# Optimization experiments

Hardware: AMD Instinct MI355X
Metric: run time of the kernel (lower is better)

## Reference

```python
import jax, jax.numpy as jnp
import numpy as np

B, T, N, H, P = 16, 64, 512, 128, 12


def _laplacian_with_self_loop(adj):
    a = adj + jnp.eye(adj.shape[0], dtype=adj.dtype)
    d_inv_sqrt = 1.0 / jnp.sqrt(a.sum(axis=1))
    return a * d_inv_sqrt[:, None] * d_inv_sqrt[None, :]


def setup_inputs() -> dict:
    key = jax.random.key(0)
    ks = jax.random.split(key, 10)
    inputs = jax.random.normal(ks[0], (B, T, N), dtype=jnp.float32)
    adj = jax.random.uniform(ks[1], (N, N), dtype=jnp.float32)
    adj = (adj + adj.T) * 0.5
    laplacian = _laplacian_with_self_loop(adj)

    def xavier(k, shape):
        fan_in, fan_out = shape[0], shape[1]
        lim = np.sqrt(6.0 / (fan_in + fan_out))
        return jax.random.uniform(k, shape, jnp.float32, -lim, lim)

    W1 = xavier(ks[2], (H + 1, 2 * H))      # graph_conv1 weights
    b1 = jnp.ones((2 * H,), jnp.float32)    # bias init 1.0
    W2 = xavier(ks[3], (H + 1, H))          # graph_conv2 weights
    b2 = jnp.zeros((H,), jnp.float32)
    att_w1 = xavier(ks[4], (H, 1))
    att_w2 = xavier(ks[5], (N, 1))
    att_w3 = xavier(ks[6], (N, 1))
    att_b1 = jnp.zeros((1,), jnp.float32)
    att_b2 = jnp.zeros((1,), jnp.float32)
    att_b3 = jnp.zeros((1,), jnp.float32)
    W_out = xavier(ks[7], (T, P))
    b_out = jnp.zeros((P,), jnp.float32)
    return dict(inputs=inputs, laplacian=laplacian, W1=W1, b1=b1, W2=W2, b2=b2,
                att_w1=att_w1, att_w2=att_w2, att_w3=att_w3,
                att_b1=att_b1, att_b2=att_b2, att_b3=att_b3,
                W_out=W_out, b_out=b_out)


def reference(inputs, laplacian, W1, b1, W2, b2,
              att_w1, att_w2, att_w3, att_b1, att_b2, att_b3,
              W_out, b_out):
    Bs, Ts, Ns = inputs.shape
    Hs = W2.shape[1]

    def graph_conv(x_t, h_flat, W, b):
        # x_t: [B,N]; h_flat: [B, N*H]
        h = h_flat.reshape(Bs, Ns, Hs)
        conc = jnp.concatenate([x_t[..., None], h], axis=-1)     # [B,N,H+1]
        agg = jnp.einsum('mn,bnc->bmc', laplacian, conc)          # [B,N,H+1]
        out = agg @ W + b                                         # [B,N,O]
        return out.reshape(Bs, -1)                                # [B,N*O] (flattened, matching torch)

    def step(h_flat, x_t):
        ru = jax.nn.sigmoid(graph_conv(x_t, h_flat, W1, b1))      # [B, N*2H]
        r, u = jnp.split(ru, 2, axis=1)                            # split on flattened dim (faithful)
        c = jnp.tanh(graph_conv(x_t, r * h_flat, W2, b2))          # [B, N*H]
        new_h = u * h_flat + (1.0 - u) * c
        return new_h, new_h

    h0 = jnp.zeros((Bs, Ns * Hs), inputs.dtype)
    _, hs = jax.lax.scan(step, h0, jnp.moveaxis(inputs, 1, 0))     # [T,B,N*H]
    hidden_states = jnp.moveaxis(hs, 0, 1).reshape(Bs, Ts, Ns, Hs)

    # SelfAttention: project H->1, then N->1 per (b,t), softmax over T
    hs1 = hidden_states.reshape(-1, Hs) @ att_w1 + att_b1          # [B*T*N, 1]
    f = (hs1.reshape(-1, Ns) @ att_w2 + att_b2).reshape(Bs, Ts)
    g = (hs1.reshape(-1, Ns) @ att_w3 + att_b3).reshape(Bs, Ts)
    beta = jax.nn.softmax(g * f, axis=-1)                          # [B,T]
    context = beta[:, :, None] * hs1.reshape(Bs, Ts, Ns)           # [B,T,N]

    context = context.transpose(0, 2, 1)                           # [B,N,T]
    Ps = W_out.shape[1]
    out = (context.reshape(-1, Ts) @ W_out + b_out).reshape(Bs, Ns, Ps)
    return out.transpose(0, 2, 1)                                  # [B,pre_len,N]
```

## Files before the change

### kernel.cpp

```cpp
#include <hip/hip_runtime.h>
#include <math.h>

#define B_ 16
#define T_ 64
#define N_ 512
#define H_ 128
#define P_ 12
#define NH 65536

__global__ __launch_bounds__(512) void lx_kernel(const float* __restrict__ x,
                                                 const float* __restrict__ L,
                                                 float* __restrict__ Lx) {
    __shared__ __align__(16) float xs[2][N_];
    const int r0 = blockIdx.x * 2;
    const int tid = threadIdx.x;
    for (int j = 0; j < 2; ++j)
        xs[j][tid] = x[(size_t)(r0 + j) * N_ + tid];
    __syncthreads();
    float a0 = 0.f, a1 = 0.f;
    const int m = tid;
#pragma unroll 8
    for (int n = 0; n < N_; ++n) {
        float lv = L[(size_t)n * N_ + m];
        a0 += xs[0][n] * lv;
        a1 += xs[1][n] * lv;
    }
    Lx[(size_t)(r0 + 0) * N_ + m] = a0;
    Lx[(size_t)(r0 + 1) * N_ + m] = a1;
}

#define FMA4(dst, a, hv)                                                      \
    dst[0] += (a) * (hv).x; dst[1] += (a) * (hv).y;                           \
    dst[2] += (a) * (hv).z; dst[3] += (a) * (hv).w;

__global__ __launch_bounds__(512) void gc1_kernel(
    const float* __restrict__ L, const float* __restrict__ Hprev,
    const float* __restrict__ Lx, const float* __restrict__ W1,
    const float* __restrict__ b1, float* __restrict__ rh,
    float* __restrict__ u, int t) {
    __shared__ __align__(16) float Ht[2][32][H_];
    union LW {
        float Lt[2][32][20];
        float Wt[16][260];
    };
    __shared__ __align__(16) LW sm;
    __shared__ __align__(16) float Zb[16][H_];

    const int tid = threadIdx.x;
    const int b = blockIdx.x & 15;
    const int m0 = (blockIdx.x >> 4) * 16;
    const float* __restrict__ Hb = Hprev + (size_t)b * NH;

    const int hrow = tid >> 5, hcol = (tid & 31) * 4;
    const int lm = tid >> 5, lk = tid & 31;

    {
        *(float4*)&Ht[0][hrow][hcol] = *(const float4*)&Hb[(size_t)hrow * H_ + hcol];
        *(float4*)&Ht[0][hrow + 16][hcol] =
            *(const float4*)&Hb[(size_t)(hrow + 16) * H_ + hcol];
        sm.Lt[0][lk][lm] = L[(size_t)(m0 + lm) * N_ + lk];
    }
    __syncthreads();

    const int g = tid >> 6;
    const int l = tid & 63;
    const int ty = l >> 4;
    const int tx = l & 15;
    const int ma0 = ty * 4;
    const int ca0 = tx * 4, cb0 = 64 + tx * 4;

    float acc[4][2][4] = {};

    for (int kc = 0; kc < 16; ++kc) {
        const int bi = kc & 1, bj = bi ^ 1;
        float4 p0, p1;
        float pl;
        if (kc < 15) {
            const size_t kb = (size_t)(kc + 1) * 32;
            p0 = *(const float4*)&Hb[(kb + hrow) * H_ + hcol];
            p1 = *(const float4*)&Hb[(kb + hrow + 16) * H_ + hcol];
            pl = L[(size_t)(m0 + lm) * N_ + kb + lk];
        }
#pragma unroll
        for (int kk = 0; kk < 4; ++kk) {
            const int k = g * 4 + kk;
            const float4 la = *(const float4*)&sm.Lt[bi][k][ma0];
            const float4 h0 = *(const float4*)&Ht[bi][k][ca0];
            const float4 h1 = *(const float4*)&Ht[bi][k][cb0];
            FMA4(acc[0][0], la.x, h0) FMA4(acc[0][1], la.x, h1)
            FMA4(acc[1][0], la.y, h0) FMA4(acc[1][1], la.y, h1)
            FMA4(acc[2][0], la.z, h0) FMA4(acc[2][1], la.z, h1)
            FMA4(acc[3][0], la.w, h0) FMA4(acc[3][1], la.w, h1)
        }
        if (kc < 15) {
            *(float4*)&Ht[bj][hrow][hcol] = p0;
            *(float4*)&Ht[bj][hrow + 16][hcol] = p1;
            sm.Lt[bj][lk][lm] = pl;
        }
        __syncthreads();
    }

    for (int r = 0; r < 8; ++r) {
        if (g == r) {
#pragma unroll
            for (int i = 0; i < 4; ++i) {
#pragma unroll
                for (int v = 0; v < 2; ++v) {
                    const int c = v ? cb0 : ca0;
                    float4* zp = (float4*)&Zb[ma0 + i][c];
                    if (r == 0) {
                        *zp = make_float4(acc[i][v][0], acc[i][v][1],
                                          acc[i][v][2], acc[i][v][3]);
                    } else {
                        float4 z = *zp;
                        *zp = make_float4(z.x + acc[i][v][0], z.y + acc[i][v][1],
                                          z.z + acc[i][v][2], z.w + acc[i][v][3]);
                    }
                }
            }
        }
        __syncthreads();
    }

    const int to = tid & 63, tm = tid >> 6;
    const int o0 = to * 4;
    float a2[2][4] = {};
    const int wr = tid >> 5, wc = (tid & 31) * 4;

    for (int ck = 0; ck < 8; ++ck) {
        *(float4*)&sm.Wt[wr][wc] =
            *(const float4*)&W1[(size_t)(1 + ck * 16 + wr) * 256 + wc];
        *(float4*)&sm.Wt[wr][wc + 128] =
            *(const float4*)&W1[(size_t)(1 + ck * 16 + wr) * 256 + wc + 128];
        __syncthreads();
#pragma unroll
        for (int ch4 = 0; ch4 < 4; ++ch4) {
            const float4 w0v = *(const float4*)&sm.Wt[ch4 * 4 + 0][o0];
            const float4 w1v = *(const float4*)&sm.Wt[ch4 * 4 + 1][o0];
            const float4 w2v = *(const float4*)&sm.Wt[ch4 * 4 + 2][o0];
            const float4 w3v = *(const float4*)&sm.Wt[ch4 * 4 + 3][o0];
            const int cc = ck * 16 + ch4 * 4;
#pragma unroll
            for (int i = 0; i < 2; ++i) {
                const float4 zv = *(const float4*)&Zb[tm + 8 * i][cc];
                a2[i][0] += zv.x * w0v.x + zv.y * w1v.x + zv.z * w2v.x + zv.w * w3v.x;
                a2[i][1] += zv.x * w0v.y + zv.y * w1v.y + zv.z * w2v.y + zv.w * w3v.y;
                a2[i][2] += zv.x * w0v.z + zv.y * w1v.z + zv.z * w2v.z + zv.w * w3v.z;
                a2[i][3] += zv.x * w0v.w + zv.y * w1v.w + zv.z * w2v.w + zv.w * w3v.w;
            }
        }
        __syncthreads();
    }

    const float4 w0r = *(const float4*)&W1[o0];
    const float4 bbv = *(const float4*)&b1[o0];
    const float* __restrict__ LxRow = Lx + ((size_t)b * T_ + t) * N_ + m0;
    float* __restrict__ rhB = rh + (size_t)b * NH;
    float* __restrict__ uB = u + (size_t)b * NH;
    const bool isR = (m0 < 256);
#pragma unroll
    for (int i = 0; i < 2; ++i) {
        const int mi = tm + 8 * i;
        const float lx = LxRow[mi];
        float v0 = a2[i][0] + lx * w0r.x + bbv.x;
        float v1 = a2[i][1] + lx * w0r.y + bbv.y;
        float v2 = a2[i][2] + lx * w0r.z + bbv.z;
        float v3 = a2[i][3] + lx * w0r.w + bbv.w;
        float s0 = 1.f / (1.f + expf(-v0));
        float s1 = 1.f / (1.f + expf(-v1));
        float s2 = 1.f / (1.f + expf(-v2));
        float s3 = 1.f / (1.f + expf(-v3));
        const int fl = (m0 + mi) * 256 + o0;
        if (isR) {
            float4 hv = *(const float4*)&Hb[fl];
            *(float4*)&rhB[fl] = make_float4(s0 * hv.x, s1 * hv.y, s2 * hv.z, s3 * hv.w);
        } else {
            *(float4*)&uB[fl - NH] = make_float4(s0, s1, s2, s3);
        }
    }
}

__global__ __launch_bounds__(512) void gc2a_kernel(
    const float* __restrict__ L, const float* __restrict__ rh,
    float* __restrict__ Z) {
    __shared__ __align__(16) float Ht[2][32][H_];
    __shared__ __align__(16) float Lt[2][32][20];
    __shared__ __align__(16) float Zb[16][H_];

    const int tid = threadIdx.x;
    const int b = blockIdx.x & 15;
    const int m0 = (blockIdx.x >> 4) * 16;
    const float* __restrict__ Rb = rh + (size_t)b * NH;

    const int hrow = tid >> 5, hcol = (tid & 31) * 4;
    const int lm = tid >> 5, lk = tid & 31;

    {
        *(float4*)&Ht[0][hrow][hcol] = *(const float4*)&Rb[(size_t)hrow * H_ + hcol];
        *(float4*)&Ht[0][hrow + 16][hcol] =
            *(const float4*)&Rb[(size_t)(hrow + 16) * H_ + hcol];
        Lt[0][lk][lm] = L[(size_t)(m0 + lm) * N_ + lk];
    }
    __syncthreads();

    const int g = tid >> 6;
    const int l = tid & 63;
    const int ty = l >> 4;
    const int tx = l & 15;
    const int ma0 = ty * 4;
    const int ca0 = tx * 4, cb0 = 64 + tx * 4;

    float acc[4][2][4] = {};

    for (int kc = 0; kc < 16; ++kc) {
        const int bi = kc & 1, bj = bi ^ 1;
        float4 p0, p1;
        float pl;
        if (kc < 15) {
            const size_t kb = (size_t)(kc + 1) * 32;
            p0 = *(const float4*)&Rb[(kb + hrow) * H_ + hcol];
            p1 = *(const float4*)&Rb[(kb + hrow + 16) * H_ + hcol];
            pl = L[(size_t)(m0 + lm) * N_ + kb + lk];
        }
#pragma unroll
        for (int kk = 0; kk < 4; ++kk) {
            const int k = g * 4 + kk;
            const float4 la = *(const float4*)&Lt[bi][k][ma0];
            const float4 h0 = *(const float4*)&Ht[bi][k][ca0];
            const float4 h1 = *(const float4*)&Ht[bi][k][cb0];
            FMA4(acc[0][0], la.x, h0) FMA4(acc[0][1], la.x, h1)
            FMA4(acc[1][0], la.y, h0) FMA4(acc[1][1], la.y, h1)
            FMA4(acc[2][0], la.z, h0) FMA4(acc[2][1], la.z, h1)
            FMA4(acc[3][0], la.w, h0) FMA4(acc[3][1], la.w, h1)
        }
        if (kc < 15) {
            *(float4*)&Ht[bj][hrow][hcol] = p0;
            *(float4*)&Ht[bj][hrow + 16][hcol] = p1;
            Lt[bj][lk][lm] = pl;
        }
        __syncthreads();
    }

    for (int r = 0; r < 8; ++r) {
        if (g == r) {
#pragma unroll
            for (int i = 0; i < 4; ++i) {
#pragma unroll
                for (int v = 0; v < 2; ++v) {
                    const int c = v ? cb0 : ca0;
                    float4* zp = (float4*)&Zb[ma0 + i][c];
                    if (r == 0) {
                        *zp = make_float4(acc[i][v][0], acc[i][v][1],
                                          acc[i][v][2], acc[i][v][3]);
                    } else {
                        float4 z = *zp;
                        *zp = make_float4(z.x + acc[i][v][0], z.y + acc[i][v][1],
                                          z.z + acc[i][v][2], z.w + acc[i][v][3]);
                    }
                }
            }
        }
        __syncthreads();
    }

    {
        const int zr = tid >> 5, zc = (tid & 31) * 4;
        *(float4*)&Z[((size_t)b * NH) + (size_t)(m0 + zr) * H_ + zc] =
            *(const float4*)&Zb[zr][zc];
    }
}

__global__ __launch_bounds__(256) void gc2b_kernel(
    const float* __restrict__ Hprev, const float* __restrict__ u,
    const float* __restrict__ Lx, const float* __restrict__ W2,
    const float* __restrict__ b2, const float* __restrict__ aw1,
    const float* __restrict__ ab1, float* __restrict__ Hnew,
    float* __restrict__ hs1, int t) {
    __shared__ __align__(16) float Zs[8][H_];
    __shared__ __align__(16) float Wt[16][H_];

    const int tid = threadIdx.x;
    const int b = blockIdx.x & 15;
    const int m0 = (blockIdx.x >> 4) * 8;
    const size_t gbase = (size_t)b * NH + (size_t)m0 * H_;

    const int row = tid >> 5;
    const int o0 = (tid & 31) * 4;

    *(float4*)&Zs[row][o0] = *(const float4*)&Hnew[gbase + (size_t)row * H_ + o0];

    float a2[4] = {0.f, 0.f, 0.f, 0.f};

#pragma unroll 1
    for (int ck = 0; ck < 8; ++ck) {
        __syncthreads();
        *(float4*)&Wt[row][o0] =
            *(const float4*)&W2[(size_t)(1 + ck * 16 + row) * H_ + o0];
        *(float4*)&Wt[row + 8][o0] =
            *(const float4*)&W2[(size_t)(1 + ck * 16 + row + 8) * H_ + o0];
        __syncthreads();
#pragma unroll
        for (int ch4 = 0; ch4 < 4; ++ch4) {
            const float4 w0v = *(const float4*)&Wt[ch4 * 4 + 0][o0];
            const float4 w1v = *(const float4*)&Wt[ch4 * 4 + 1][o0];
            const float4 w2v = *(const float4*)&Wt[ch4 * 4 + 2][o0];
            const float4 w3v = *(const float4*)&Wt[ch4 * 4 + 3][o0];
            const float4 zv = *(const float4*)&Zs[row][ck * 16 + ch4 * 4];
            a2[0] += zv.x * w0v.x + zv.y * w1v.x + zv.z * w2v.x + zv.w * w3v.x;
            a2[1] += zv.x * w0v.y + zv.y * w1v.y + zv.z * w2v.y + zv.w * w3v.y;
            a2[2] += zv.x * w0v.z + zv.y * w1v.z + zv.z * w2v.z + zv.w * w3v.z;
            a2[3] += zv.x * w0v.w + zv.y * w1v.w + zv.z * w2v.w + zv.w * w3v.w;
        }
    }

    const float4 w0r = *(const float4*)&W2[o0];
    const float4 bbv = *(const float4*)&b2[o0];
    const float4 awv = *(const float4*)&aw1[o0];
    const int m = m0 + row;
    const float lx = Lx[((size_t)b * T_ + t) * N_ + m];

    float c0 = tanhf(a2[0] + lx * w0r.x + bbv.x);
    float c1 = tanhf(a2[1] + lx * w0r.y + bbv.y);
    float c2 = tanhf(a2[2] + lx * w0r.z + bbv.z);
    float c3 = tanhf(a2[3] + lx * w0r.w + bbv.w);

    const size_t fl = gbase + (size_t)row * H_ + o0;
    const float4 uv = *(const float4*)&u[fl];
    const float4 hp = *(const float4*)&Hprev[fl];
    const float h0 = uv.x * hp.x + (1.f - uv.x) * c0;
    const float h1 = uv.y * hp.y + (1.f - uv.y) * c1;
    const float h2 = uv.z * hp.z + (1.f - uv.z) * c2;
    const float h3 = uv.w * hp.w + (1.f - uv.w) * c3;
    *(float4*)&Hnew[fl] = make_float4(h0, h1, h2, h3);

    float part = h0 * awv.x + h1 * awv.y + h2 * awv.z + h3 * awv.w;
#pragma unroll
    for (int off = 16; off; off >>= 1) part += __shfl_xor(part, off);
    if ((tid & 31) == 0)
        hs1[((size_t)b * T_ + t) * N_ + m] = part + ab1[0];
}

__global__ __launch_bounds__(64) void att_beta_kernel(
    const float* __restrict__ hs1, const float* __restrict__ aw2,
    const float* __restrict__ aw3, const float* __restrict__ ab2,
    const float* __restrict__ ab3, float* __restrict__ beta) {
    const int b = blockIdx.x;
    const int t = threadIdx.x;
    const float* __restrict__ row = hs1 + ((size_t)b * T_ + t) * N_;
    float f = 0.f, g = 0.f;
    for (int n = 0; n < N_; n += 4) {
        float4 hv = *(const float4*)&row[n];
        float4 w2v = *(const float4*)&aw2[n];
        float4 w3v = *(const float4*)&aw3[n];
        f += hv.x * w2v.x + hv.y * w2v.y + hv.z * w2v.z + hv.w * w2v.w;
        g += hv.x * w3v.x + hv.y * w3v.y + hv.z * w3v.z + hv.w * w3v.w;
    }
    f += ab2[0];
    g += ab3[0];
    float s = f * g;
    float mx = s;
    for (int off = 32; off; off >>= 1) mx = fmaxf(mx, __shfl_xor(mx, off));
    float e = expf(s - mx);
    float sum = e;
    for (int off = 32; off; off >>= 1) sum += __shfl_xor(sum, off);
    beta[b * T_ + t] = e / sum;
}

__global__ __launch_bounds__(256) void att_out_kernel(
    const float* __restrict__ hs1, const float* __restrict__ beta,
    const float* __restrict__ Wout, const float* __restrict__ bout,
    float* __restrict__ out) {
    __shared__ float bs[T_];
    __shared__ float ws[T_][P_];
    const int b = blockIdx.x;
    const int tid = threadIdx.x;
    if (tid < T_) bs[tid] = beta[b * T_ + tid];
    for (int i = tid; i < T_ * P_; i += 256) ws[i / P_][i % P_] = Wout[i];
    __syncthreads();
    for (int nn = 0; nn < 2; ++nn) {
        const int n = tid + nn * 256;
        float acc[P_];
#pragma unroll
        for (int p = 0; p < P_; ++p) acc[p] = bout[p];
        for (int t = 0; t < T_; ++t) {
            float v = bs[t] * hs1[((size_t)b * T_ + t) * N_ + n];
#pragma unroll
            for (int p = 0; p < P_; ++p) acc[p] += v * ws[t][p];
        }
#pragma unroll
        for (int p = 0; p < P_; ++p) out[((size_t)b * P_ + p) * N_ + n] = acc[p];
    }
}

extern "C" void kernel_launch(void* const* d_in, const int* in_sizes, int n_in,
                              void* d_out, int out_size, void* d_ws, size_t ws_size,
                              hipStream_t stream) {
    const float* x = (const float*)d_in[0];
    const float* L = (const float*)d_in[1];
    const float* W1 = (const float*)d_in[2];
    const float* b1 = (const float*)d_in[3];
    const float* W2 = (const float*)d_in[4];
    const float* b2 = (const float*)d_in[5];
    const float* aw1 = (const float*)d_in[6];
    const float* aw2 = (const float*)d_in[7];
    const float* aw3 = (const float*)d_in[8];
    const float* ab1 = (const float*)d_in[9];
    const float* ab2 = (const float*)d_in[10];
    const float* ab3 = (const float*)d_in[11];
    const float* Wout = (const float*)d_in[12];
    const float* bout = (const float*)d_in[13];
    float* out = (float*)d_out;

    float* ws = (float*)d_ws;
    float* Lx = ws;
    float* hs1 = Lx + B_ * T_ * N_;
    float* hb0 = hs1 + B_ * T_ * N_;
    float* hb1 = hb0 + (size_t)B_ * NH;
    float* rh = hb1 + (size_t)B_ * NH;
    float* u = rh + (size_t)B_ * NH;
    float* beta = u + (size_t)B_ * NH;
    (void)in_sizes; (void)n_in; (void)out_size; (void)ws_size;

    hipMemsetAsync(hb0, 0, (size_t)B_ * NH * sizeof(float), stream);
    lx_kernel<<<512, 512, 0, stream>>>(x, L, Lx);

    for (int t = 0; t < T_; ++t) {
        float* hp = (t & 1) ? hb1 : hb0;
        float* hn = (t & 1) ? hb0 : hb1;
        gc1_kernel<<<512, 512, 0, stream>>>(L, hp, Lx, W1, b1, rh, u, t);
        gc2a_kernel<<<512, 512, 0, stream>>>(L, rh, hn);
        gc2b_kernel<<<1024, 256, 0, stream>>>(hp, u, Lx, W2, b2, aw1, ab1,
                                              hn, hs1, t);
    }
    att_beta_kernel<<<16, 64, 0, stream>>>(hs1, aw2, aw3, ab2, ab3, beta);
    att_out_kernel<<<16, 256, 0, stream>>>(hs1, beta, Wout, bout, out);
}
```

Baseline: 4.001 ms.

## Reorder second graph conv as L·(rh·W2) and fuse the GRU epilogue

The second graph convolution now multiplies r*h by W2 first, in a new per-node kernel, and then applies the Laplacian to the result. This lets the Laplacian GEMM kernel finish with the tanh, GRU update and attention projection directly from shared memory. The intermediate Z no longer makes a global round trip, and the Laplacian GEMM's output feeds the epilogue directly, at the cost of an extra Y buffer. A padding shared array is added, which appears meant to limit occupancy or change the LDS footprint.

```diff
diff --git a/kernel.cpp b/kernel.cpp
--- a/kernel.cpp
+++ b/kernel.cpp
@@ -180,25 +180,77 @@
     }
 }
 
-__global__ __launch_bounds__(512) void gc2a_kernel(
-    const float* __restrict__ L, const float* __restrict__ rh,
-    float* __restrict__ Z) {
+__global__ __launch_bounds__(256) void y_kernel(
+    const float* __restrict__ rh, const float* __restrict__ W2,
+    float* __restrict__ Y) {
+    __shared__ __align__(16) float Zs[8][H_];
+    __shared__ __align__(16) float Wt[16][H_];
+
+    const int tid = threadIdx.x;
+    const int b = blockIdx.x & 15;
+    const int n0 = (blockIdx.x >> 4) * 8;
+    const size_t gbase = (size_t)b * NH + (size_t)n0 * H_;
+
+    const int row = tid >> 5;
+    const int o0 = (tid & 31) * 4;
+
+    *(float4*)&Zs[row][o0] = *(const float4*)&rh[gbase + (size_t)row * H_ + o0];
+
+    float a2[4] = {0.f, 0.f, 0.f, 0.f};
+
+#pragma unroll 1
+    for (int ck = 0; ck < 8; ++ck) {
+        __syncthreads();
+        *(float4*)&Wt[row][o0] =
+            *(const float4*)&W2[(size_t)(1 + ck * 16 + row) * H_ + o0];
+        *(float4*)&Wt[row + 8][o0] =
+            *(const float4*)&W2[(size_t)(1 + ck * 16 + row + 8) * H_ + o0];
+        __syncthreads();
+#pragma unroll
+        for (int ch4 = 0; ch4 < 4; ++ch4) {
+            const float4 w0v = *(const float4*)&Wt[ch4 * 4 + 0][o0];
+            const float4 w1v = *(const float4*)&Wt[ch4 * 4 + 1][o0];
+            const float4 w2v = *(const float4*)&Wt[ch4 * 4 + 2][o0];
+            const float4 w3v = *(const float4*)&Wt[ch4 * 4 + 3][o0];
+            const float4 zv = *(const float4*)&Zs[row][ck * 16 + ch4 * 4];
+            a2[0] += zv.x * w0v.x + zv.y * w1v.x + zv.z * w2v.x + zv.w * w3v.x;
+            a2[1] += zv.x * w0v.y + zv.y * w1v.y + zv.z * w2v.y + zv.w * w3v.y;
+            a2[2] += zv.x * w0v.z + zv.y * w1v.z + zv.z * w2v.z + zv.w * w3v.z;
+            a2[3] += zv.x * w0v.w + zv.y * w1v.w + zv.z * w2v.w + zv.w * w3v.w;
+        }
+    }
+
+    *(float4*)&Y[gbase + (size_t)row * H_ + o0] =
+        make_float4(a2[0], a2[1], a2[2], a2[3]);
+}
+
+__global__ __launch_bounds__(512) void gcz_kernel(
+    const float* __restrict__ L, const float* __restrict__ Y,
+    const float* __restrict__ Hprev, const float* __restrict__ u,
+    const float* __restrict__ Lx, const float* __restrict__ W2,
+    const float* __restrict__ b2, const float* __restrict__ aw1,
+    const float* __restrict__ ab1, float* __restrict__ Hnew,
+    float* __restrict__ hs1, int t) {
     __shared__ __align__(16) float Ht[2][32][H_];
     __shared__ __align__(16) float Lt[2][32][20];
     __shared__ __align__(16) float Zb[16][H_];
+    __shared__ __align__(16) float pad_[2880];
 
     const int tid = threadIdx.x;
+    if (tid < 16) pad_[tid] = 0.f;
+    asm volatile("" ::: "memory");
+
     const int b = blockIdx.x & 15;
     const int m0 = (blockIdx.x >> 4) * 16;
-    const float* __restrict__ Rb = rh + (size_t)b * NH;
+    const float* __restrict__ Yb = Y + (size_t)b * NH;
 
     const int hrow = tid >> 5, hcol = (tid & 31) * 4;
     const int lm = tid >> 5, lk = tid & 31;
 
     {
-        *(float4*)&Ht[0][hrow][hcol] = *(const float4*)&Rb[(size_t)hrow * H_ + hcol];
+        *(float4*)&Ht[0][hrow][hcol] = *(const float4*)&Yb[(size_t)hrow * H_ + hcol];
         *(float4*)&Ht[0][hrow + 16][hcol] =
-            *(const float4*)&Rb[(size_t)(hrow + 16) * H_ + hcol];
+            *(const float4*)&Yb[(size_t)(hrow + 16) * H_ + hcol];
         Lt[0][lk][lm] = L[(size_t)(m0 + lm) * N_ + lk];
     }
     __syncthreads();
@@ -218,8 +270,8 @@
         float pl;
         if (kc < 15) {
             const size_t kb = (size_t)(kc + 1) * 32;
-            p0 = *(const float4*)&Rb[(kb + hrow) * H_ + hcol];
-            p1 = *(const float4*)&Rb[(kb + hrow + 16) * H_ + hcol];
+            p0 = *(const float4*)&Yb[(kb + hrow) * H_ + hcol];
+            p1 = *(const float4*)&Yb[(kb + hrow + 16) * H_ + hcol];
             pl = L[(size_t)(m0 + lm) * N_ + kb + lk];
         }
 #pragma unroll
@@ -263,68 +315,20 @@
         __syncthreads();
     }
 
-    {
-        const int zr = tid >> 5, zc = (tid & 31) * 4;
-        *(float4*)&Z[((size_t)b * NH) + (size_t)(m0 + zr) * H_ + zc] =
-            *(const float4*)&Zb[zr][zc];
-    }
-}
-
-__global__ __launch_bounds__(256) void gc2b_kernel(
-    const float* __restrict__ Hprev, const float* __restrict__ u,
-    const float* __restrict__ Lx, const float* __restrict__ W2,
-    const float* __restrict__ b2, const float* __restrict__ aw1,
-    const float* __restrict__ ab1, float* __restrict__ Hnew,
-    float* __restrict__ hs1, int t) {
-    __shared__ __align__(16) float Zs[8][H_];
-    __shared__ __align__(16) float Wt[16][H_];
-
-    const int tid = threadIdx.x;
-    const int b = blockIdx.x & 15;
-    const int m0 = (blockIdx.x >> 4) * 8;
-    const size_t gbase = (size_t)b * NH + (size_t)m0 * H_;
-
-    const int row = tid >> 5;
-    const int o0 = (tid & 31) * 4;
-
-    *(float4*)&Zs[row][o0] = *(const float4*)&Hnew[gbase + (size_t)row * H_ + o0];
-
-    float a2[4] = {0.f, 0.f, 0.f, 0.f};
-
-#pragma unroll 1
-    for (int ck = 0; ck < 8; ++ck) {
-        __syncthreads();
-        *(float4*)&Wt[row][o0] =
-            *(const float4*)&W2[(size_t)(1 + ck * 16 + row) * H_ + o0];
-        *(float4*)&Wt[row + 8][o0] =
-            *(const float4*)&W2[(size_t)(1 + ck * 16 + row + 8) * H_ + o0];
-        __syncthreads();
-#pragma unroll
-        for (int ch4 = 0; ch4 < 4; ++ch4) {
-            const float4 w0v = *(const float4*)&Wt[ch4 * 4 + 0][o0];
-            const float4 w1v = *(const float4*)&Wt[ch4 * 4 + 1][o0];
-            const float4 w2v = *(const float4*)&Wt[ch4 * 4 + 2][o0];
-            const float4 w3v = *(const float4*)&Wt[ch4 * 4 + 3][o0];
-            const float4 zv = *(const float4*)&Zs[row][ck * 16 + ch4 * 4];
-            a2[0] += zv.x * w0v.x + zv.y * w1v.x + zv.z * w2v.x + zv.w * w3v.x;
-            a2[1] += zv.x * w0v.y + zv.y * w1v.y + zv.z * w2v.y + zv.w * w3v.y;
-            a2[2] += zv.x * w0v.z + zv.y * w1v.z + zv.z * w2v.z + zv.w * w3v.z;
-            a2[3] += zv.x * w0v.w + zv.y * w1v.w + zv.z * w2v.w + zv.w * w3v.w;
-        }
-    }
-
-    const float4 w0r = *(const float4*)&W2[o0];
-    const float4 bbv = *(const float4*)&b2[o0];
-    const float4 awv = *(const float4*)&aw1[o0];
-    const int m = m0 + row;
-    const float lx = Lx[((size_t)b * T_ + t) * N_ + m];
-
-    float c0 = tanhf(a2[0] + lx * w0r.x + bbv.x);
-    float c1 = tanhf(a2[1] + lx * w0r.y + bbv.y);
-    float c2 = tanhf(a2[2] + lx * w0r.z + bbv.z);
-    float c3 = tanhf(a2[3] + lx * w0r.w + bbv.w);
-
-    const size_t fl = gbase + (size_t)row * H_ + o0;
+    const int zr = tid >> 5;
+    const int zc = (tid & 31) * 4;
+    const float4 zv = *(const float4*)&Zb[zr][zc];
+    const float4 w0r = *(const float4*)&W2[zc];
+    const float4 bbv = *(const float4*)&b2[zc];
+    const float4 awv = *(const float4*)&aw1[zc];
+    const float lx = Lx[((size_t)b * T_ + t) * N_ + m0 + zr];
+
+    float c0 = tanhf(zv.x + lx * w0r.x + bbv.x);
+    float c1 = tanhf(zv.y + lx * w0r.y + bbv.y);
+    float c2 = tanhf(zv.z + lx * w0r.z + bbv.z);
+    float c3 = tanhf(zv.w + lx * w0r.w + bbv.w);
+
+    const size_t fl = (size_t)b * NH + (size_t)(m0 + zr) * H_ + zc;
     const float4 uv = *(const float4*)&u[fl];
     const float4 hp = *(const float4*)&Hprev[fl];
     const float h0 = uv.x * hp.x + (1.f - uv.x) * c0;
@@ -337,7 +341,7 @@
 #pragma unroll
     for (int off = 16; off; off >>= 1) part += __shfl_xor(part, off);
     if ((tid & 31) == 0)
-        hs1[((size_t)b * T_ + t) * N_ + m] = part + ab1[0];
+        hs1[((size_t)b * T_ + t) * N_ + m0 + zr] = part + ab1[0];
 }
 
 __global__ __launch_bounds__(64) void att_beta_kernel(
@@ -418,7 +422,8 @@
     float* hb1 = hb0 + (size_t)B_ * NH;
     float* rh = hb1 + (size_t)B_ * NH;
     float* u = rh + (size_t)B_ * NH;
-    float* beta = u + (size_t)B_ * NH;
+    float* Ybuf = u + (size_t)B_ * NH;
+    float* beta = Ybuf + (size_t)B_ * NH;
     (void)in_sizes; (void)n_in; (void)out_size; (void)ws_size;
 
     hipMemsetAsync(hb0, 0, (size_t)B_ * NH * sizeof(float), stream);
@@ -428,9 +433,9 @@
         float* hp = (t & 1) ? hb1 : hb0;
         float* hn = (t & 1) ? hb0 : hb1;
         gc1_kernel<<<512, 512, 0, stream>>>(L, hp, Lx, W1, b1, rh, u, t);
-        gc2a_kernel<<<512, 512, 0, stream>>>(L, rh, hn);
-        gc2b_kernel<<<1024, 256, 0, stream>>>(hp, u, Lx, W2, b2, aw1, ab1,
-                                              hn, hs1, t);
+        y_kernel<<<1024, 256, 0, stream>>>(rh, W2, Ybuf);
+        gcz_kernel<<<512, 512, 0, stream>>>(L, Ybuf, hp, u, Lx, W2, b2, aw1,
+                                            ab1, hn, hs1, t);
     }
     att_beta_kernel<<<16, 64, 0, stream>>>(hs1, aw2, aw3, ab2, ab3, beta);
     att_out_kernel<<<16, 256, 0, stream>>>(hs1, beta, Wout, bout, out);
```

New measurement: 4.154 ms. 1.04x slower.
